# Kernel optimization log

Measured on AMD Instinct MI355X. Metric: run time of the kernel, lower is better.

Reference implementation:

```python
import jax, jax.numpy as jnp
import numpy as np

B, N, D = 64, 576, 768   # batch, num_patches (24x24), embed_dim
K = 1024                 # n_pairs
NUM_TARGETS = 2


def setup_inputs() -> dict:
    key = jax.random.key(0)
    k1, k2, k3, k4 = jax.random.split(key, 4)
    z = jax.random.normal(k1, (B, N, D), dtype=jnp.float32)
    indices = jax.random.randint(k2, (B, K, 2), 0, N, dtype=jnp.int64)
    # head params: nn.Linear(2*embed_dim, num_targets)
    W = jax.random.normal(k3, (2 * D, NUM_TARGETS), dtype=jnp.float32) * 0.02
    b_head = jax.random.normal(k4, (NUM_TARGETS,), dtype=jnp.float32) * 0.02
    return {"z": z, "indices": indices, "W": W, "b_head": b_head}


def reference(z, indices, W, b_head):
    b, n, d = z.shape
    k = indices.shape[1]
    # index_pairs: gather both patches of each pair -> [b, k, 2, d]
    batch_idx = jnp.arange(b)[:, None, None]            # [b,1,1]
    z_pairs = z[batch_idx, indices]                     # [b, k, 2, d]
    # pairwise_mlp head: concat pair along feature dim, tiny linear
    out = z_pairs.reshape(b, k, 2 * d) @ W + b_head     # [b, k, num_targets]
    return out, indices
```

## Files before the change

### kernel.cpp

```cpp
#include <hip/hip_runtime.h>

#define BB 64
#define NN 576
#define DD 768
#define KK 1024
#define ROWS (BB * NN)
#define PAIRS (BB * KK)

#define K1_BLOCKS 2304
#define TPB 256

__device__ float4 g_P[ROWS];

__device__ __forceinline__ float4 rowdot(const float4 v[3],
                                         const float2 wa[3][4],
                                         const float2 wb[3][4]) {
    float s0 = 0.f, s1 = 0.f, s2 = 0.f, s3 = 0.f;
#pragma unroll
    for (int j = 0; j < 3; ++j) {
        const float e0 = v[j].x, e1 = v[j].y, e2 = v[j].z, e3 = v[j].w;
        s0 = fmaf(e0, wa[j][0].x, s0);
        s0 = fmaf(e1, wa[j][1].x, s0);
        s0 = fmaf(e2, wa[j][2].x, s0);
        s0 = fmaf(e3, wa[j][3].x, s0);
        s1 = fmaf(e0, wa[j][0].y, s1);
        s1 = fmaf(e1, wa[j][1].y, s1);
        s1 = fmaf(e2, wa[j][2].y, s1);
        s1 = fmaf(e3, wa[j][3].y, s1);
        s2 = fmaf(e0, wb[j][0].x, s2);
        s2 = fmaf(e1, wb[j][1].x, s2);
        s2 = fmaf(e2, wb[j][2].x, s2);
        s2 = fmaf(e3, wb[j][3].x, s2);
        s3 = fmaf(e0, wb[j][0].y, s3);
        s3 = fmaf(e1, wb[j][1].y, s3);
        s3 = fmaf(e2, wb[j][2].y, s3);
        s3 = fmaf(e3, wb[j][3].y, s3);
    }
    return make_float4(s0, s1, s2, s3);
}

__device__ __forceinline__ void bfly2(float4& p, float4& q) {
#pragma unroll
    for (int off = 32; off > 0; off >>= 1) {
        p.x += __shfl_xor(p.x, off, 64);
        q.x += __shfl_xor(q.x, off, 64);
        p.y += __shfl_xor(p.y, off, 64);
        q.y += __shfl_xor(q.y, off, 64);
        p.z += __shfl_xor(p.z, off, 64);
        q.z += __shfl_xor(q.z, off, 64);
        p.w += __shfl_xor(p.w, off, 64);
        q.w += __shfl_xor(q.w, off, 64);
    }
}

__global__ __launch_bounds__(TPB, 4)
void partvit_proj(const float* __restrict__ z, const float* __restrict__ W) {
    const int lane = threadIdx.x & 63;
    const int wave = threadIdx.x >> 6;

    const int rbase = (blockIdx.x * 4 + wave) * 4;

    const float4* __restrict__ z4 = (const float4*)z;
    float4 v[4][3];
#pragma unroll
    for (int rr = 0; rr < 4; ++rr)
#pragma unroll
        for (int j = 0; j < 3; ++j)
            v[rr][j] = z4[(size_t)(rbase + rr) * 192 + j * 64 + lane];

    const float2* __restrict__ W2 = (const float2*)W;
    float2 wa[3][4], wb[3][4];
#pragma unroll
    for (int j = 0; j < 3; ++j)
#pragma unroll
        for (int c = 0; c < 4; ++c) {
            const int d = j * 256 + (lane << 2) + c;
            wa[j][c] = W2[d];
            wb[j][c] = W2[d + DD];
        }

    float4 p0 = rowdot(v[0], wa, wb);
    float4 p1 = rowdot(v[1], wa, wb);
    bfly2(p0, p1);
    if (lane == 0)      g_P[rbase + 0] = p0;
    else if (lane == 1) g_P[rbase + 1] = p1;

    float4 p2 = rowdot(v[2], wa, wb);
    float4 p3 = rowdot(v[3], wa, wb);
    bfly2(p2, p3);
    if (lane == 0)      g_P[rbase + 2] = p2;
    else if (lane == 1) g_P[rbase + 3] = p3;
}

__global__ __launch_bounds__(TPB) void partvit_pairs(const int* __restrict__ idx,
                                                     const float* __restrict__ bh,
                                                     float* __restrict__ out) {
    const int t = blockIdx.x * blockDim.x + threadIdx.x;
    if (t >= PAIRS) return;
    const int2 id = ((const int2*)idx)[t];
    const int i0 = min(max(id.x, 0), NN - 1);
    const int i1 = min(max(id.y, 0), NN - 1);
    const int b = t >> 10;
    const float4 p0 = g_P[b * NN + i0];
    const float4 p1 = g_P[b * NN + i1];
    const float b0 = bh[0], b1 = bh[1];
    ((float2*)out)[t] = make_float2(p0.x + p1.z + b0, p0.y + p1.w + b1);
    ((float2*)out)[PAIRS + t] = make_float2((float)id.x, (float)id.y);
}

extern "C" void kernel_launch(void* const* d_in, const int* in_sizes, int n_in,
                              void* d_out, int out_size, void* d_ws, size_t ws_size,
                              hipStream_t stream) {
    const float* z   = (const float*)d_in[0];
    const int*   idx = (const int*)d_in[1];
    const float* W   = (const float*)d_in[2];
    const float* bh  = (const float*)d_in[3];
    float*       out = (float*)d_out;
    (void)d_ws; (void)ws_size; (void)in_sizes; (void)n_in; (void)out_size;

    partvit_proj<<<K1_BLOCKS, TPB, 0, stream>>>(z, W);
    partvit_pairs<<<PAIRS / TPB, TPB, 0, stream>>>(idx, bh, out);
}
```

Before: 166.4 us.

## Fuse projection and pair gather into one producer-consumer kernel

Merges the two launches into a single grid. Producer blocks compute the per-row projections and bump a global completion counter. Consumer blocks, placed after them, write the index output early and then spin until every producer has finished before gathering. This removes one kernel launch and the gap between kernels. In exchange it relies on block scheduling order, uses a monotonically growing counter across calls, and has a spin timeout that could let consumers read stale data.

```diff
diff --git a/kernel.cpp b/kernel.cpp
--- a/kernel.cpp
+++ b/kernel.cpp
@@ -7,10 +7,14 @@
 #define ROWS (BB * NN)
 #define PAIRS (BB * KK)
 
-#define K1_BLOCKS 2304
+#define PROD_BLOCKS 2304
+#define CONS_BLOCKS 256
 #define TPB 256
+#define PAIRS_PER_CONS (PAIRS / CONS_BLOCKS)
 
-__device__ float4 g_P[ROWS];
+__device__ float4   g_P[ROWS];
+__device__ unsigned g_done = 0;
+__device__ unsigned g_rseq = 0;
 
 __device__ __forceinline__ float4 rowdot(const float4 v[3],
                                          const float2 wa[3][4],
@@ -54,58 +58,80 @@
 }
 
 __global__ __launch_bounds__(TPB, 4)
-void partvit_proj(const float* __restrict__ z, const float* __restrict__ W) {
-    const int lane = threadIdx.x & 63;
-    const int wave = threadIdx.x >> 6;
+void partvit_pc(const float* __restrict__ z,
+                const int* __restrict__ idx,
+                const float* __restrict__ W,
+                const float* __restrict__ bh,
+                float* __restrict__ out) {
+    if (blockIdx.x < PROD_BLOCKS) {
+        const int lane = threadIdx.x & 63;
+        const int wave = threadIdx.x >> 6;
+        const int rbase = (blockIdx.x * 4 + wave) * 4;
 
-    const int rbase = (blockIdx.x * 4 + wave) * 4;
+        const float4* __restrict__ z4 = (const float4*)z;
+        float4 v[4][3];
+#pragma unroll
+        for (int rr = 0; rr < 4; ++rr)
+#pragma unroll
+            for (int j = 0; j < 3; ++j)
+                v[rr][j] = z4[(size_t)(rbase + rr) * 192 + j * 64 + lane];
 
-    const float4* __restrict__ z4 = (const float4*)z;
-    float4 v[4][3];
-#pragma unroll
-    for (int rr = 0; rr < 4; ++rr)
+        const float2* __restrict__ W2 = (const float2*)W;
+        float2 wa[3][4], wb[3][4];
 #pragma unroll
         for (int j = 0; j < 3; ++j)
-            v[rr][j] = z4[(size_t)(rbase + rr) * 192 + j * 64 + lane];
+#pragma unroll
+            for (int c = 0; c < 4; ++c) {
+                const int d = j * 256 + (lane << 2) + c;
+                wa[j][c] = W2[d];
+                wb[j][c] = W2[d + DD];
+            }
 
-    const float2* __restrict__ W2 = (const float2*)W;
-    float2 wa[3][4], wb[3][4];
-#pragma unroll
-    for (int j = 0; j < 3; ++j)
-#pragma unroll
-        for (int c = 0; c < 4; ++c) {
-            const int d = j * 256 + (lane << 2) + c;
-            wa[j][c] = W2[d];
-            wb[j][c] = W2[d + DD];
+        float4 p0 = rowdot(v[0], wa, wb);
+        float4 p1 = rowdot(v[1], wa, wb);
+        bfly2(p0, p1);
+        if (lane == 0)      g_P[rbase + 0] = p0;
+        else if (lane == 1) g_P[rbase + 1] = p1;
+
+        float4 p2 = rowdot(v[2], wa, wb);
+        float4 p3 = rowdot(v[3], wa, wb);
+        bfly2(p2, p3);
+        if (lane == 0)      g_P[rbase + 2] = p2;
+        else if (lane == 1) g_P[rbase + 3] = p3;
+
+        __syncthreads();
+        if (threadIdx.x == 0) {
+            __threadfence();
+            atomicAdd(&g_done, 1u);
         }
+    } else {
+        const int c = blockIdx.x - PROD_BLOCKS;
+        const int t = c * PAIRS_PER_CONS + (int)threadIdx.x;
 
-    float4 p0 = rowdot(v[0], wa, wb);
-    float4 p1 = rowdot(v[1], wa, wb);
-    bfly2(p0, p1);
-    if (lane == 0)      g_P[rbase + 0] = p0;
-    else if (lane == 1) g_P[rbase + 1] = p1;
+        const int2 id = ((const int2*)idx)[t];
+        ((float2*)out)[PAIRS + t] = make_float2((float)id.x, (float)id.y);
+        const float b0 = bh[0], b1 = bh[1];
+        const int i0 = min(max(id.x, 0), NN - 1);
+        const int i1 = min(max(id.y, 0), NN - 1);
+        const int b = t >> 10;
 
-    float4 p2 = rowdot(v[2], wa, wb);
-    float4 p3 = rowdot(v[3], wa, wb);
-    bfly2(p2, p3);
-    if (lane == 0)      g_P[rbase + 2] = p2;
-    else if (lane == 1) g_P[rbase + 3] = p3;
-}
+        if (threadIdx.x == 0) {
+            const unsigned seq = atomicAdd(&g_rseq, 1u);
+            const unsigned target = (seq / CONS_BLOCKS + 1u) * PROD_BLOCKS;
+            unsigned spins = 0;
+            while (__hip_atomic_load(&g_done, __ATOMIC_RELAXED,
+                                     __HIP_MEMORY_SCOPE_AGENT) < target) {
+                if (++spins > (1u << 20)) break;
+                __builtin_amdgcn_s_sleep(8);
+            }
+            __threadfence();
+        }
+        __syncthreads();
 
-__global__ __launch_bounds__(TPB) void partvit_pairs(const int* __restrict__ idx,
-                                                     const float* __restrict__ bh,
-                                                     float* __restrict__ out) {
-    const int t = blockIdx.x * blockDim.x + threadIdx.x;
-    if (t >= PAIRS) return;
-    const int2 id = ((const int2*)idx)[t];
-    const int i0 = min(max(id.x, 0), NN - 1);
-    const int i1 = min(max(id.y, 0), NN - 1);
-    const int b = t >> 10;
-    const float4 p0 = g_P[b * NN + i0];
-    const float4 p1 = g_P[b * NN + i1];
-    const float b0 = bh[0], b1 = bh[1];
-    ((float2*)out)[t] = make_float2(p0.x + p1.z + b0, p0.y + p1.w + b1);
-    ((float2*)out)[PAIRS + t] = make_float2((float)id.x, (float)id.y);
+        const float4 p0 = g_P[b * NN + i0];
+        const float4 p1 = g_P[b * NN + i1];
+        ((float2*)out)[t] = make_float2(p0.x + p1.z + b0, p0.y + p1.w + b1);
+    }
 }
 
 extern "C" void kernel_launch(void* const* d_in, const int* in_sizes, int n_in,
@@ -118,6 +144,5 @@
     float*       out = (float*)d_out;
     (void)d_ws; (void)ws_size; (void)in_sizes; (void)n_in; (void)out_size;
 
-    partvit_proj<<<K1_BLOCKS, TPB, 0, stream>>>(z, W);
-    partvit_pairs<<<PAIRS / TPB, TPB, 0, stream>>>(idx, bh, out);
+    partvit_pc<<<PROD_BLOCKS + CONS_BLOCKS, TPB, 0, stream>>>(z, idx, W, bh, out);
 }
```

After: 319.8 us. 92.2% more time.

## Stream z rows through double-buffered LDS via global_load_lds in projection kernel

Applied to the files above, without the earlier changes.

The projection kernel no longer loads four rows per wave straight into registers. Each block now streams 16 rows in four tiles through a two-stage LDS buffer, filled by asynchronous global_load_lds 16-byte DMA loads. The next tile's load is issued while the current row's dot product and wave reduction run. The aim is to hide HBM latency, but each wave now has fewer loads in flight, and every tile adds a block-wide barrier. Correct ordering of the LDS DMA before the reads also depends on the compiler inserting the right waits.

```diff
diff --git a/kernel.cpp b/kernel.cpp
--- a/kernel.cpp
+++ b/kernel.cpp
@@ -1,4 +1,5 @@
 #include <hip/hip_runtime.h>
+#include <stdint.h>
 
 #define BB 64
 #define NN 576
@@ -7,10 +8,20 @@
 #define ROWS (BB * NN)
 #define PAIRS (BB * KK)
 
-#define K1_BLOCKS 2304
 #define TPB 256
+#define TILE_ROWS 4
+#define TILES 4
+#define K1_BLOCKS (ROWS / (TILES * TILE_ROWS))
 
 __device__ float4 g_P[ROWS];
+
+__device__ __forceinline__ void gload_lds16(const float4* g, float4* l) {
+    __builtin_amdgcn_global_load_lds(
+        (const __attribute__((address_space(1))) void*)(uintptr_t)g,
+        (__attribute__((address_space(3))) void*)(uintptr_t)(
+            (char*)l - (char*)nullptr ? (void*)l : (void*)l),
+        16, 0, 0);
+}
 
 __device__ __forceinline__ float4 rowdot(const float4 v[3],
                                          const float2 wa[3][4],
@@ -39,34 +50,14 @@
     return make_float4(s0, s1, s2, s3);
 }
 
-__device__ __forceinline__ void bfly2(float4& p, float4& q) {
-#pragma unroll
-    for (int off = 32; off > 0; off >>= 1) {
-        p.x += __shfl_xor(p.x, off, 64);
-        q.x += __shfl_xor(q.x, off, 64);
-        p.y += __shfl_xor(p.y, off, 64);
-        q.y += __shfl_xor(q.y, off, 64);
-        p.z += __shfl_xor(p.z, off, 64);
-        q.z += __shfl_xor(q.z, off, 64);
-        p.w += __shfl_xor(p.w, off, 64);
-        q.w += __shfl_xor(q.w, off, 64);
-    }
-}
-
 __global__ __launch_bounds__(TPB, 4)
 void partvit_proj(const float* __restrict__ z, const float* __restrict__ W) {
+    __shared__ float4 buf[2][TILE_ROWS * 192];
     const int lane = threadIdx.x & 63;
     const int wave = threadIdx.x >> 6;
-
-    const int rbase = (blockIdx.x * 4 + wave) * 4;
+    const int rbase = blockIdx.x * (TILES * TILE_ROWS);
 
     const float4* __restrict__ z4 = (const float4*)z;
-    float4 v[4][3];
-#pragma unroll
-    for (int rr = 0; rr < 4; ++rr)
-#pragma unroll
-        for (int j = 0; j < 3; ++j)
-            v[rr][j] = z4[(size_t)(rbase + rr) * 192 + j * 64 + lane];
 
     const float2* __restrict__ W2 = (const float2*)W;
     float2 wa[3][4], wb[3][4];
@@ -79,17 +70,43 @@
             wb[j][c] = W2[d + DD];
         }
 
-    float4 p0 = rowdot(v[0], wa, wb);
-    float4 p1 = rowdot(v[1], wa, wb);
-    bfly2(p0, p1);
-    if (lane == 0)      g_P[rbase + 0] = p0;
-    else if (lane == 1) g_P[rbase + 1] = p1;
+#pragma unroll
+    for (int k = 0; k < 3; ++k) {
+        const int chunk = wave * 3 + k;
+        gload_lds16(&z4[(size_t)rbase * 192 + chunk * 64 + lane],
+                    &buf[0][chunk * 64]);
+    }
+    __syncthreads();
 
-    float4 p2 = rowdot(v[2], wa, wb);
-    float4 p3 = rowdot(v[3], wa, wb);
-    bfly2(p2, p3);
-    if (lane == 0)      g_P[rbase + 2] = p2;
-    else if (lane == 1) g_P[rbase + 3] = p3;
+#pragma unroll
+    for (int t = 0; t < TILES; ++t) {
+        if (t + 1 < TILES) {
+            const size_t base = ((size_t)rbase + (size_t)(t + 1) * TILE_ROWS) * 192;
+#pragma unroll
+            for (int k = 0; k < 3; ++k) {
+                const int chunk = wave * 3 + k;
+                gload_lds16(&z4[base + chunk * 64 + lane],
+                            &buf[(t + 1) & 1][chunk * 64]);
+            }
+        }
+
+        float4 v[3];
+#pragma unroll
+        for (int j = 0; j < 3; ++j)
+            v[j] = buf[t & 1][wave * 192 + j * 64 + lane];
+
+        float4 p = rowdot(v, wa, wb);
+#pragma unroll
+        for (int off = 32; off > 0; off >>= 1) {
+            p.x += __shfl_xor(p.x, off, 64);
+            p.y += __shfl_xor(p.y, off, 64);
+            p.z += __shfl_xor(p.z, off, 64);
+            p.w += __shfl_xor(p.w, off, 64);
+        }
+        if (lane == 0) g_P[rbase + t * TILE_ROWS + wave] = p;
+
+        __syncthreads();
+    }
 }
 
 __global__ __launch_bounds__(TPB) void partvit_pairs(const int* __restrict__ idx,
```

Measured after the change: 170.0 us. +2.2%, slower.
